# Kernel optimization log

Hardware: AMD Instinct MI355X
Metric: run time of the kernel (lower is better)

The kernel has to match this reference:

```python
import jax, jax.numpy as jnp
import numpy as np

RES = 2048
IN = 3
OUT = 2
THRESHOLD = 1.0
BETA = 0.9
SPECTRAL_RADIUS = 0.9


def _make_W(rng):
    # random recurrent matrix scaled to target spectral radius (power iteration estimate)
    W = rng.standard_normal((RES, RES)).astype(np.float32)
    v = rng.standard_normal(RES).astype(np.float32)
    lam = 1.0
    for _ in range(100):
        v = W @ v
        lam = np.linalg.norm(v)
        v = v / (lam + 1e-12)
    return W * (SPECTRAL_RADIUS / lam)


def _xavier(rng, fan_out, fan_in):
    bound = np.sqrt(6.0 / (fan_in + fan_out))
    return rng.uniform(-bound, bound, (fan_out, fan_in)).astype(np.float32)


def setup_inputs() -> dict:
    key = jax.random.key(0)
    rng = np.random.default_rng(42)
    x = jax.random.normal(key, (200, 256, IN), dtype=jnp.float32)
    W = jnp.asarray(_make_W(rng))            # [RES, RES] recurrent weights
    Win = jnp.asarray(_xavier(rng, RES, IN))  # [RES, IN]  input_layer.weight
    Wout = jnp.asarray(_xavier(rng, OUT, RES))  # [OUT, RES] readout.weight
    return {"x": x, "W": W, "Win": Win, "Wout": Wout}


def reference(x, W, Win, Wout):
    seq_len, batch, _ = x.shape
    res = W.shape[0]

    def step(carry, x_t):
        V, S = carry
        # leaky integrate: input current + recurrent current
        V_new = BETA * V + x_t @ Win.T + S @ W  # [batch, res]
        S_new = (V_new >= THRESHOLD).astype(V.dtype)
        V_new = V_new * (1.0 - S_new)  # reset_mechanism == 'zero'
        return (V_new, S_new), S_new

    init = (jnp.zeros((batch, res), x.dtype), jnp.zeros((batch, res), x.dtype))
    _, spk_rec = jax.lax.scan(step, init, x)  # [seq, batch, res]
    spk_avg = spk_rec[-10:].mean(axis=0)       # [batch, res]
    logits = spk_avg @ Wout.T                  # [batch, out]
    return spk_rec, logits
```

## Files before the change

### kernel.cpp

```cpp
#include <hip/hip_runtime.h>


#define SEQ    200
#define BATCH  256
#define NRES   2048
#define NTHR   512
#define BETA_F 0.9f

__global__ __launch_bounds__(NTHR, 1) void snn_reservoir_kernel(
    const float* __restrict__ x,
    const float* __restrict__ W,
    const float* __restrict__ Win,
    const float* __restrict__ Wout,
    float* __restrict__ out)
{
    const int b    = blockIdx.x;
    const int tid  = threadIdx.x;
    const int lane = tid & 63;
    const int wid  = tid >> 6;
    const int n0   = tid << 2;

    __shared__ float4 sx[SEQ];
    __shared__ unsigned long long smask[2][32];
    __shared__ int   scum[2];
    __shared__ float red[2][8];
    __shared__ int   anyflag;

    for (int t = tid; t < SEQ; t += NTHR) {
        const float* p = x + (size_t)t * (BATCH * 3) + b * 3;
        sx[t] = make_float4(p[0], p[1], p[2], 0.0f);
    }
    if (tid == 0) anyflag = 0;

    float wi[4][3];
    #pragma unroll
    for (int j = 0; j < 4; ++j) {
        const float* p = Win + (size_t)(n0 + j) * 3;
        wi[j][0] = p[0]; wi[j][1] = p[1]; wi[j][2] = p[2];
    }

    float V[4]  = {0.f, 0.f, 0.f, 0.f};
    int   cnt[4] = {0, 0, 0, 0};

    __syncthreads();

    {
        float* po = out + (size_t)b * NRES + n0;
        bool spiked = false;
        #pragma unroll 2
        for (int t = 0; t < SEQ; ++t) {
            const float4 xv = sx[t];
            float4 sp;
            #pragma unroll
            for (int j = 0; j < 4; ++j) {
                const float cur = fmaf(xv.x, wi[j][0],
                                  fmaf(xv.y, wi[j][1], xv.z * wi[j][2]));
                V[j] = fmaf(BETA_F, V[j], cur);
                const bool s = (V[j] >= 1.0f);
                spiked |= s;
                V[j] = s ? 0.f : V[j];
                ((float*)&sp)[j] = s ? 1.f : 0.f;
                if (t >= SEQ - 10) cnt[j] += (int)s;
            }
            *(float4*)po = sp;
            po += BATCH * NRES;
        }
        const unsigned long long bal = __ballot(spiked);
        if (lane == 0 && bal != 0ull) atomicOr(&anyflag, 1);
    }
    __syncthreads();

    if (anyflag) {
        #pragma unroll
        for (int j = 0; j < 4; ++j) { V[j] = 0.f; cnt[j] = 0; }
        if (tid < 64) smask[tid >> 5][tid & 31] = 0ull;
        if (tid < 2)  scum[tid] = 0;
        __syncthreads();

        int seen[2] = {0, 0};
        float* po = out + (size_t)b * NRES + n0;
        for (int t = 0; t < SEQ; ++t) {
            const int curp = t & 1, prev = curp ^ 1;
            float rec[4] = {0.f, 0.f, 0.f, 0.f};
            const int c = scum[prev];
            if (c != seen[prev]) {
                seen[prev] = c;
                #pragma unroll 1
                for (int u = 0; u < 32; ++u) {
                    unsigned long long m = smask[prev][u];
                    const int kbase = ((u >> 2) << 8) + (u & 3);
                    while (m) {
                        const int l = __builtin_ctzll(m);
                        m &= m - 1;
                        const int k = kbase + (l << 2);
                        const float4 wv = *(const float4*)(W + (size_t)k * NRES + n0);
                        rec[0] += wv.x; rec[1] += wv.y;
                        rec[2] += wv.z; rec[3] += wv.w;
                    }
                }
            }
            const float4 xv = sx[t];
            float4 sp;
            int pc = 0;
            unsigned long long bj[4];
            #pragma unroll
            for (int j = 0; j < 4; ++j) {
                const float cur = fmaf(xv.x, wi[j][0],
                                  fmaf(xv.y, wi[j][1], xv.z * wi[j][2])) + rec[j];
                V[j] = fmaf(BETA_F, V[j], cur);
                const bool s = (V[j] >= 1.0f);
                V[j] = s ? 0.f : V[j];
                ((float*)&sp)[j] = s ? 1.f : 0.f;
                if (t >= SEQ - 10) cnt[j] += (int)s;
                bj[j] = __ballot(s);
                pc += (int)s;
            }
            *(float4*)po = sp;
            po += BATCH * NRES;
            if (lane == 0) {
                #pragma unroll
                for (int j = 0; j < 4; ++j) smask[curp][(wid << 2) + j] = bj[j];
            }
            if (lane == 0) {
                int wpc = 0;
                #pragma unroll
                for (int j = 0; j < 4; ++j) wpc += __popcll(bj[j]);
                if (wpc) atomicAdd(&scum[curp], wpc);
            }
            __syncthreads();
        }
    }

    const float4 w0 = *(const float4*)(Wout + n0);
    const float4 w1 = *(const float4*)(Wout + NRES + n0);
    float p0 = cnt[0] * 0.1f * w0.x + cnt[1] * 0.1f * w0.y +
               cnt[2] * 0.1f * w0.z + cnt[3] * 0.1f * w0.w;
    float p1 = cnt[0] * 0.1f * w1.x + cnt[1] * 0.1f * w1.y +
               cnt[2] * 0.1f * w1.z + cnt[3] * 0.1f * w1.w;
    #pragma unroll
    for (int off = 32; off > 0; off >>= 1) {
        p0 += __shfl_down(p0, off);
        p1 += __shfl_down(p1, off);
    }
    if (lane == 0) { red[0][wid] = p0; red[1][wid] = p1; }
    __syncthreads();
    if (tid == 0) {
        float q0 = 0.f, q1 = 0.f;
        #pragma unroll
        for (int i = 0; i < 8; ++i) { q0 += red[0][i]; q1 += red[1][i]; }
        const size_t loff = (size_t)SEQ * BATCH * NRES;
        out[loff + b * 2 + 0] = q0;
        out[loff + b * 2 + 1] = q1;
    }
}

extern "C" void kernel_launch(void* const* d_in, const int* in_sizes, int n_in,
                              void* d_out, int out_size, void* d_ws, size_t ws_size,
                              hipStream_t stream) {
    const float* x    = (const float*)d_in[0];
    const float* W    = (const float*)d_in[1];
    const float* Win  = (const float*)d_in[2];
    const float* Wout = (const float*)d_in[3];
    float* out = (float*)d_out;
    hipLaunchKernelGGL(snn_reservoir_kernel, dim3(BATCH), dim3(NTHR), 0, stream,
                       x, W, Win, Wout, out);
}
```

Measured before the change: 423.7 us.

## Split spike-free scan into checkpointed scan and time-parallel write kernels

A first kernel runs the input-only leaky-integrate recurrence per batch row, saving membrane checkpoints every 8 steps to workspace and recording whether any neuron spiked. A second kernel with 800 blocks reads those checkpoints and replays 8-step chunks for 8 batch rows each, writing the spike tensor in parallel across time. The goal is to spread the large output write over many more blocks than the original 256 serial ones. The cost is roughly 52MB of extra checkpoint traffic and a second launch. If any spike occurs, it falls back to the sequential recurrent path, and it uses a monolithic kernel when the workspace is too small.

```diff
diff --git a/kernel.cpp b/kernel.cpp
--- a/kernel.cpp
+++ b/kernel.cpp
@@ -4,133 +4,211 @@
 #define SEQ    200
 #define BATCH  256
 #define NRES   2048
-#define NTHR   512
+#define K_CHK  8
+#define C_CHK  25
+#define M_SUB  32
+#define BPB    8
 #define BETA_F 0.9f
 
-__global__ __launch_bounds__(NTHR, 1) void snn_reservoir_kernel(
-    const float* __restrict__ x,
-    const float* __restrict__ W,
-    const float* __restrict__ Win,
-    const float* __restrict__ Wout,
-    float* __restrict__ out)
+#define WS_CKPT_F4OFF 256
+#define WS_NEED (1024 + (size_t)C_CHK * BATCH * NRES * 4)
+
+__global__ __launch_bounds__(512, 1) void snn_scan_kernel(
+    const float* __restrict__ x, const float* __restrict__ Win,
+    float* __restrict__ ws)
 {
-    const int b    = blockIdx.x;
-    const int tid  = threadIdx.x;
-    const int lane = tid & 63;
-    const int wid  = tid >> 6;
-    const int n0   = tid << 2;
-
+    const int b = blockIdx.x, tid = threadIdx.x, n0 = tid << 2;
+    __shared__ float4 sx[SEQ];
+    __shared__ int wor[8];
+
+    for (int t = tid; t < SEQ; t += 512) {
+        const float* p = x + (size_t)t * (BATCH * 3) + b * 3;
+        sx[t] = make_float4(p[0], p[1], p[2], 0.f);
+    }
+    const float* wp = Win + (size_t)n0 * 3;
+    const float4 wa = *(const float4*)wp;
+    const float4 wb = *(const float4*)(wp + 4);
+    const float4 wc = *(const float4*)(wp + 8);
+    const float wi[4][3] = {{wa.x, wa.y, wa.z}, {wa.w, wb.x, wb.y},
+                            {wb.z, wb.w, wc.x}, {wc.y, wc.z, wc.w}};
+    float V[4] = {0.f, 0.f, 0.f, 0.f};
+    bool spiked = false;
+    float* ck = ws + WS_CKPT_F4OFF;
+    __syncthreads();
+
+    for (int t = 0; t < SEQ; ++t) {
+        if ((t & 7) == 0) {
+            const int c = t >> 3;
+            *(float4*)(ck + (size_t)(c * BATCH + b) * NRES + n0) =
+                make_float4(V[0], V[1], V[2], V[3]);
+        }
+        const float4 xv = sx[t];
+        #pragma unroll
+        for (int j = 0; j < 4; ++j) {
+            const float cur = fmaf(xv.x, wi[j][0], fmaf(xv.y, wi[j][1], xv.z * wi[j][2]));
+            V[j] = fmaf(BETA_F, V[j], cur);
+            const bool s = (V[j] >= 1.0f);
+            spiked |= s;
+            V[j] = s ? 0.f : V[j];
+        }
+    }
+    const unsigned long long bal = __ballot(spiked);
+    if ((tid & 63) == 0) wor[tid >> 6] = (bal != 0ull) ? 1 : 0;
+    __syncthreads();
+    if (tid == 0) {
+        int f = 0;
+        #pragma unroll
+        for (int i = 0; i < 8; ++i) f |= wor[i];
+        ((int*)ws)[b] = f;
+    }
+}
+
+__global__ __launch_bounds__(512, 1) void snn_write_kernel(
+    const float* __restrict__ x, const float* __restrict__ W,
+    const float* __restrict__ Win, const float* __restrict__ Wout,
+    const float* __restrict__ ws, float* __restrict__ out)
+{
+    const int tid = threadIdx.x, lane = tid & 63, wid = tid >> 6;
+    __shared__ int sflag;
+    __shared__ float4 sxc[K_CHK][BPB];
     __shared__ float4 sx[SEQ];
     __shared__ unsigned long long smask[2][32];
-    __shared__ int   scum[2];
+    __shared__ int scum[2];
     __shared__ float red[2][8];
-    __shared__ int   anyflag;
-
-    for (int t = tid; t < SEQ; t += NTHR) {
+
+    if (tid == 0) sflag = 0;
+    __syncthreads();
+    {
+        const int f = (tid < BATCH) ? ((const int*)ws)[tid] : 0;
+        if (__ballot(f != 0)) { if (lane == 0) atomicOr(&sflag, 1); }
+    }
+    __syncthreads();
+
+    if (!sflag) {
+        const int c  = blockIdx.x >> 5;
+        const int m  = blockIdx.x & 31;
+        const int b0 = m * BPB;
+        const int t0 = c * K_CHK;
+        const int n0 = tid << 2;
+
+        if (tid < K_CHK * BPB) {
+            const int tl = tid >> 3, bl = tid & 7;
+            const float* p = x + (size_t)(t0 + tl) * (BATCH * 3) + (b0 + bl) * 3;
+            sxc[tl][bl] = make_float4(p[0], p[1], p[2], 0.f);
+        }
+        const float* wp = Win + (size_t)n0 * 3;
+        const float4 wa = *(const float4*)wp;
+        const float4 wb = *(const float4*)(wp + 4);
+        const float4 wc = *(const float4*)(wp + 8);
+        const float wi[4][3] = {{wa.x, wa.y, wa.z}, {wa.w, wb.x, wb.y},
+                                {wb.z, wb.w, wc.x}, {wc.y, wc.z, wc.w}};
+        __syncthreads();
+
+        unsigned sbits[BPB];
+        const float* ck = ws + WS_CKPT_F4OFF;
+        #pragma unroll
+        for (int g = 0; g < BPB; ++g) {
+            const float4 V4 = *(const float4*)(ck + (size_t)(c * BATCH + b0 + g) * NRES + n0);
+            float V[4] = {V4.x, V4.y, V4.z, V4.w};
+            unsigned bits = 0u;
+            #pragma unroll
+            for (int tl = 0; tl < K_CHK; ++tl) {
+                const float4 xv = sxc[tl][g];
+                #pragma unroll
+                for (int j = 0; j < 4; ++j) {
+                    const float cur = fmaf(xv.x, wi[j][0],
+                                      fmaf(xv.y, wi[j][1], xv.z * wi[j][2]));
+                    V[j] = fmaf(BETA_F, V[j], cur);
+                    const bool s = (V[j] >= 1.0f);
+                    bits |= (unsigned)s << (tl * 4 + j);
+                    V[j] = s ? 0.f : V[j];
+                }
+            }
+            sbits[g] = bits;
+        }
+        #pragma unroll
+        for (int tl = 0; tl < K_CHK; ++tl) {
+            float* po = out + ((size_t)(t0 + tl) * BATCH + b0) * NRES + n0;
+            #pragma unroll
+            for (int g = 0; g < BPB; ++g) {
+                const unsigned bt = sbits[g] >> (tl * 4);
+                *(float4*)(po + (size_t)g * NRES) =
+                    make_float4((bt & 1u) ? 1.f : 0.f, (bt & 2u) ? 1.f : 0.f,
+                                (bt & 4u) ? 1.f : 0.f, (bt & 8u) ? 1.f : 0.f);
+            }
+        }
+        if (blockIdx.x == 0) out[(size_t)SEQ * BATCH * NRES + tid] = 0.f;
+        return;
+    }
+
+    if (blockIdx.x >= BATCH) return;
+    const int b = blockIdx.x;
+    const int n0 = tid << 2;
+
+    for (int t = tid; t < SEQ; t += 512) {
         const float* p = x + (size_t)t * (BATCH * 3) + b * 3;
-        sx[t] = make_float4(p[0], p[1], p[2], 0.0f);
-    }
-    if (tid == 0) anyflag = 0;
-
-    float wi[4][3];
-    #pragma unroll
-    for (int j = 0; j < 4; ++j) {
-        const float* p = Win + (size_t)(n0 + j) * 3;
-        wi[j][0] = p[0]; wi[j][1] = p[1]; wi[j][2] = p[2];
-    }
-
-    float V[4]  = {0.f, 0.f, 0.f, 0.f};
-    int   cnt[4] = {0, 0, 0, 0};
-
-    __syncthreads();
-
-    {
-        float* po = out + (size_t)b * NRES + n0;
-        bool spiked = false;
-        #pragma unroll 2
-        for (int t = 0; t < SEQ; ++t) {
-            const float4 xv = sx[t];
-            float4 sp;
+        sx[t] = make_float4(p[0], p[1], p[2], 0.f);
+    }
+    if (tid < 64) smask[tid >> 5][tid & 31] = 0ull;
+    if (tid < 2)  scum[tid] = 0;
+    const float* wp = Win + (size_t)n0 * 3;
+    const float4 wa = *(const float4*)wp;
+    const float4 wb = *(const float4*)(wp + 4);
+    const float4 wc = *(const float4*)(wp + 8);
+    const float wi[4][3] = {{wa.x, wa.y, wa.z}, {wa.w, wb.x, wb.y},
+                            {wb.z, wb.w, wc.x}, {wc.y, wc.z, wc.w}};
+    float V[4] = {0.f, 0.f, 0.f, 0.f};
+    int cnt[4] = {0, 0, 0, 0};
+    __syncthreads();
+
+    int seen[2] = {0, 0};
+    float* po = out + (size_t)b * NRES + n0;
+    for (int t = 0; t < SEQ; ++t) {
+        const int curp = t & 1, prev = curp ^ 1;
+        float rec[4] = {0.f, 0.f, 0.f, 0.f};
+        const int csp = scum[prev];
+        if (csp != seen[prev]) {
+            seen[prev] = csp;
+            #pragma unroll 1
+            for (int u = 0; u < 32; ++u) {
+                unsigned long long mm = smask[prev][u];
+                const int kbase = ((u >> 2) << 8) + (u & 3);
+                while (mm) {
+                    const int l = __builtin_ctzll(mm);
+                    mm &= mm - 1;
+                    const int k = kbase + (l << 2);
+                    const float4 wv = *(const float4*)(W + (size_t)k * NRES + n0);
+                    rec[0] += wv.x; rec[1] += wv.y; rec[2] += wv.z; rec[3] += wv.w;
+                }
+            }
+        }
+        const float4 xv = sx[t];
+        float4 sp;
+        unsigned long long bj[4];
+        #pragma unroll
+        for (int j = 0; j < 4; ++j) {
+            const float cur = fmaf(xv.x, wi[j][0],
+                              fmaf(xv.y, wi[j][1], xv.z * wi[j][2])) + rec[j];
+            V[j] = fmaf(BETA_F, V[j], cur);
+            const bool s = (V[j] >= 1.0f);
+            V[j] = s ? 0.f : V[j];
+            ((float*)&sp)[j] = s ? 1.f : 0.f;
+            if (t >= SEQ - 10) cnt[j] += (int)s;
+            bj[j] = __ballot(s);
+        }
+        *(float4*)po = sp;
+        po += BATCH * NRES;
+        if (lane == 0) {
+            int wpc = 0;
             #pragma unroll
             for (int j = 0; j < 4; ++j) {
-                const float cur = fmaf(xv.x, wi[j][0],
-                                  fmaf(xv.y, wi[j][1], xv.z * wi[j][2]));
-                V[j] = fmaf(BETA_F, V[j], cur);
-                const bool s = (V[j] >= 1.0f);
-                spiked |= s;
-                V[j] = s ? 0.f : V[j];
-                ((float*)&sp)[j] = s ? 1.f : 0.f;
-                if (t >= SEQ - 10) cnt[j] += (int)s;
-            }
-            *(float4*)po = sp;
-            po += BATCH * NRES;
-        }
-        const unsigned long long bal = __ballot(spiked);
-        if (lane == 0 && bal != 0ull) atomicOr(&anyflag, 1);
-    }
-    __syncthreads();
-
-    if (anyflag) {
-        #pragma unroll
-        for (int j = 0; j < 4; ++j) { V[j] = 0.f; cnt[j] = 0; }
-        if (tid < 64) smask[tid >> 5][tid & 31] = 0ull;
-        if (tid < 2)  scum[tid] = 0;
+                smask[curp][(wid << 2) + j] = bj[j];
+                wpc += __popcll(bj[j]);
+            }
+            if (wpc) atomicAdd(&scum[curp], wpc);
+        }
         __syncthreads();
-
-        int seen[2] = {0, 0};
-        float* po = out + (size_t)b * NRES + n0;
-        for (int t = 0; t < SEQ; ++t) {
-            const int curp = t & 1, prev = curp ^ 1;
-            float rec[4] = {0.f, 0.f, 0.f, 0.f};
-            const int c = scum[prev];
-            if (c != seen[prev]) {
-                seen[prev] = c;
-                #pragma unroll 1
-                for (int u = 0; u < 32; ++u) {
-                    unsigned long long m = smask[prev][u];
-                    const int kbase = ((u >> 2) << 8) + (u & 3);
-                    while (m) {
-                        const int l = __builtin_ctzll(m);
-                        m &= m - 1;
-                        const int k = kbase + (l << 2);
-                        const float4 wv = *(const float4*)(W + (size_t)k * NRES + n0);
-                        rec[0] += wv.x; rec[1] += wv.y;
-                        rec[2] += wv.z; rec[3] += wv.w;
-                    }
-                }
-            }
-            const float4 xv = sx[t];
-            float4 sp;
-            int pc = 0;
-            unsigned long long bj[4];
-            #pragma unroll
-            for (int j = 0; j < 4; ++j) {
-                const float cur = fmaf(xv.x, wi[j][0],
-                                  fmaf(xv.y, wi[j][1], xv.z * wi[j][2])) + rec[j];
-                V[j] = fmaf(BETA_F, V[j], cur);
-                const bool s = (V[j] >= 1.0f);
-                V[j] = s ? 0.f : V[j];
-                ((float*)&sp)[j] = s ? 1.f : 0.f;
-                if (t >= SEQ - 10) cnt[j] += (int)s;
-                bj[j] = __ballot(s);
-                pc += (int)s;
-            }
-            *(float4*)po = sp;
-            po += BATCH * NRES;
-            if (lane == 0) {
-                #pragma unroll
-                for (int j = 0; j < 4; ++j) smask[curp][(wid << 2) + j] = bj[j];
-            }
-            if (lane == 0) {
-                int wpc = 0;
-                #pragma unroll
-                for (int j = 0; j < 4; ++j) wpc += __popcll(bj[j]);
-                if (wpc) atomicAdd(&scum[curp], wpc);
-            }
-            __syncthreads();
-        }
-    }
-
+    }
     const float4 w0 = *(const float4*)(Wout + n0);
     const float4 w1 = *(const float4*)(Wout + NRES + n0);
     float p0 = cnt[0] * 0.1f * w0.x + cnt[1] * 0.1f * w0.y +
@@ -154,6 +232,133 @@
     }
 }
 
+__global__ __launch_bounds__(512, 1) void snn_mono_kernel(
+    const float* __restrict__ x, const float* __restrict__ W,
+    const float* __restrict__ Win, const float* __restrict__ Wout,
+    float* __restrict__ out)
+{
+    const int b = blockIdx.x, tid = threadIdx.x, lane = tid & 63, wid = tid >> 6;
+    const int n0 = tid << 2;
+    __shared__ float4 sx[SEQ];
+    __shared__ unsigned long long smask[2][32];
+    __shared__ int scum[2];
+    __shared__ float red[2][8];
+    __shared__ int anyflag;
+
+    for (int t = tid; t < SEQ; t += 512) {
+        const float* p = x + (size_t)t * (BATCH * 3) + b * 3;
+        sx[t] = make_float4(p[0], p[1], p[2], 0.f);
+    }
+    if (tid == 0) anyflag = 0;
+    const float* wp = Win + (size_t)n0 * 3;
+    const float4 wa = *(const float4*)wp;
+    const float4 wb = *(const float4*)(wp + 4);
+    const float4 wc = *(const float4*)(wp + 8);
+    const float wi[4][3] = {{wa.x, wa.y, wa.z}, {wa.w, wb.x, wb.y},
+                            {wb.z, wb.w, wc.x}, {wc.y, wc.z, wc.w}};
+    float V[4] = {0.f, 0.f, 0.f, 0.f};
+    int cnt[4] = {0, 0, 0, 0};
+    __syncthreads();
+    {
+        float* po = out + (size_t)b * NRES + n0;
+        bool spiked = false;
+        for (int t = 0; t < SEQ; ++t) {
+            const float4 xv = sx[t];
+            float4 sp;
+            #pragma unroll
+            for (int j = 0; j < 4; ++j) {
+                const float cur = fmaf(xv.x, wi[j][0], fmaf(xv.y, wi[j][1], xv.z * wi[j][2]));
+                V[j] = fmaf(BETA_F, V[j], cur);
+                const bool s = (V[j] >= 1.0f);
+                spiked |= s;
+                V[j] = s ? 0.f : V[j];
+                ((float*)&sp)[j] = s ? 1.f : 0.f;
+                if (t >= SEQ - 10) cnt[j] += (int)s;
+            }
+            *(float4*)po = sp;
+            po += BATCH * NRES;
+        }
+        if (lane == 0 && __ballot(spiked) != 0ull) atomicOr(&anyflag, 1);
+    }
+    __syncthreads();
+    if (anyflag) {
+        #pragma unroll
+        for (int j = 0; j < 4; ++j) { V[j] = 0.f; cnt[j] = 0; }
+        if (tid < 64) smask[tid >> 5][tid & 31] = 0ull;
+        if (tid < 2)  scum[tid] = 0;
+        __syncthreads();
+        int seen[2] = {0, 0};
+        float* po = out + (size_t)b * NRES + n0;
+        for (int t = 0; t < SEQ; ++t) {
+            const int curp = t & 1, prev = curp ^ 1;
+            float rec[4] = {0.f, 0.f, 0.f, 0.f};
+            const int csp = scum[prev];
+            if (csp != seen[prev]) {
+                seen[prev] = csp;
+                #pragma unroll 1
+                for (int u = 0; u < 32; ++u) {
+                    unsigned long long mm = smask[prev][u];
+                    const int kbase = ((u >> 2) << 8) + (u & 3);
+                    while (mm) {
+                        const int l = __builtin_ctzll(mm);
+                        mm &= mm - 1;
+                        const int k = kbase + (l << 2);
+                        const float4 wv = *(const float4*)(W + (size_t)k * NRES + n0);
+                        rec[0] += wv.x; rec[1] += wv.y; rec[2] += wv.z; rec[3] += wv.w;
+                    }
+                }
+            }
+            const float4 xv = sx[t];
+            float4 sp;
+            unsigned long long bj[4];
+            #pragma unroll
+            for (int j = 0; j < 4; ++j) {
+                const float cur = fmaf(xv.x, wi[j][0],
+                                  fmaf(xv.y, wi[j][1], xv.z * wi[j][2])) + rec[j];
+                V[j] = fmaf(BETA_F, V[j], cur);
+                const bool s = (V[j] >= 1.0f);
+                V[j] = s ? 0.f : V[j];
+                ((float*)&sp)[j] = s ? 1.f : 0.f;
+                if (t >= SEQ - 10) cnt[j] += (int)s;
+                bj[j] = __ballot(s);
+            }
+            *(float4*)po = sp;
+            po += BATCH * NRES;
+            if (lane == 0) {
+                int wpc = 0;
+                #pragma unroll
+                for (int j = 0; j < 4; ++j) {
+                    smask[curp][(wid << 2) + j] = bj[j];
+                    wpc += __popcll(bj[j]);
+                }
+                if (wpc) atomicAdd(&scum[curp], wpc);
+            }
+            __syncthreads();
+        }
+    }
+    const float4 w0 = *(const float4*)(Wout + n0);
+    const float4 w1 = *(const float4*)(Wout + NRES + n0);
+    float p0 = cnt[0] * 0.1f * w0.x + cnt[1] * 0.1f * w0.y +
+               cnt[2] * 0.1f * w0.z + cnt[3] * 0.1f * w0.w;
+    float p1 = cnt[0] * 0.1f * w1.x + cnt[1] * 0.1f * w1.y +
+               cnt[2] * 0.1f * w1.z + cnt[3] * 0.1f * w1.w;
+    #pragma unroll
+    for (int off = 32; off > 0; off >>= 1) {
+        p0 += __shfl_down(p0, off);
+        p1 += __shfl_down(p1, off);
+    }
+    if (lane == 0) { red[0][wid] = p0; red[1][wid] = p1; }
+    __syncthreads();
+    if (tid == 0) {
+        float q0 = 0.f, q1 = 0.f;
+        #pragma unroll
+        for (int i = 0; i < 8; ++i) { q0 += red[0][i]; q1 += red[1][i]; }
+        const size_t loff = (size_t)SEQ * BATCH * NRES;
+        out[loff + b * 2 + 0] = q0;
+        out[loff + b * 2 + 1] = q1;
+    }
+}
+
 extern "C" void kernel_launch(void* const* d_in, const int* in_sizes, int n_in,
                               void* d_out, int out_size, void* d_ws, size_t ws_size,
                               hipStream_t stream) {
@@ -162,6 +367,14 @@
     const float* Win  = (const float*)d_in[2];
     const float* Wout = (const float*)d_in[3];
     float* out = (float*)d_out;
-    hipLaunchKernelGGL(snn_reservoir_kernel, dim3(BATCH), dim3(NTHR), 0, stream,
-                       x, W, Win, Wout, out);
+    if (ws_size >= WS_NEED) {
+        float* ws = (float*)d_ws;
+        hipLaunchKernelGGL(snn_scan_kernel, dim3(BATCH), dim3(512), 0, stream,
+                           x, Win, ws);
+        hipLaunchKernelGGL(snn_write_kernel, dim3(C_CHK * M_SUB), dim3(512), 0, stream,
+                           x, W, Win, Wout, ws, out);
+    } else {
+        hipLaunchKernelGGL(snn_mono_kernel, dim3(BATCH), dim3(512), 0, stream,
+                           x, W, Win, Wout, out);
+    }
 }
```

Result: slower. 468.0 us (+10.5%).
